# Kernel optimization log

Hardware: AMD Instinct MI355X
Metric: run time of the kernel (lower is better)

## Reference

```python
import jax, jax.numpy as jnp
import numpy as np

NPOINT = 2048

def setup_inputs() -> dict:
    key = jax.random.key(0)
    xyz = jax.random.normal(key, (32, 3, 65536), dtype=jnp.float32)
    return {"xyz": xyz}

def furthest_point_sampling(pts, npoint):
    # pts: [B, N, 3] -> indices [B, npoint] int32
    B, N, _ = pts.shape
    batch = jnp.arange(B)

    def step(carry, _):
        dist, farthest = carry  # dist [B,N], farthest [B]
        centroid = pts[batch, farthest]              # [B, 3]
        d = jnp.sum((pts - centroid[:, None, :]) ** 2, axis=-1)  # [B, N]
        dist = jnp.minimum(dist, d)
        nxt = jnp.argmax(dist, axis=-1).astype(jnp.int32)
        return (dist, nxt), farthest

    init = (jnp.full((B, N), 1e10, dtype=pts.dtype),
            jnp.zeros((B,), dtype=jnp.int32))
    _, idx = jax.lax.scan(step, init, None, length=npoint)
    return idx.T  # [B, npoint]

def reference(xyz):
    # xyz: [B, 3, N]; module permutes to [B, N, 3] and runs FPS
    pts = jnp.transpose(xyz, (0, 2, 1)).astype(jnp.float32)
    return furthest_point_sampling(pts, NPOINT)
```

## Files before the change

kernel.cpp:

```cpp
#include <hip/hip_runtime.h>
#include <stdint.h>

#pragma clang fp contract(off)

#define NPT      2048
#define NBATCH   32
#define NPTS     65536
#define MEMBERS  8
#define NTHREADS 512
#define CHUNK    (NPTS / MEMBERS)
#define PPT      (CHUNK / NTHREADS)
#define WPB      (NTHREADS / 64)

__device__ __forceinline__ uint32_t f2u(float f) { return __float_as_uint(f); }
__device__ __forceinline__ float u2f(uint32_t u) { return __uint_as_float(u); }

__global__ void __launch_bounds__(NTHREADS)
fps_kernel(const float* __restrict__ xyz, int* __restrict__ out,
           uint64_t* __restrict__ cand)
{
    __shared__ float    sx[CHUNK];
    __shared__ uint32_t red[WPB][2];
    __shared__ uint32_t bc[3];

    const int i = blockIdx.x;
    const int q = i >> 3;
    const int batch  = (i & 7) * 4 + (q & 3);
    const int member = q >> 2;
    const int tid  = threadIdx.x;
    const int lane = tid & 63;
    const int wv   = tid >> 6;

    const float* xb = xyz + (size_t)batch * 3 * NPTS;
    const int gbase = member * CHUNK;

    float py[PPT], pz[PPT], pd[PPT];
#pragma unroll
    for (int k = 0; k < PPT; ++k) {
        int p = tid + k * NTHREADS;
        int g = gbase + p;
        sx[p] = xb[g];
        py[k] = xb[NPTS + g];
        pz[k] = xb[2 * NPTS + g];
        pd[k] = 1e10f;
    }

    float cx = xb[0], cy = xb[NPTS], cz = xb[2 * NPTS];
    if (member == 0 && tid == 0) out[(size_t)batch * NPT] = 0;

    uint64_t* cb = cand + (size_t)batch * 2 * MEMBERS;

    for (int t = 0; t < NPT - 1; ++t) {
        float bv = -1.0f;
        int   bi = 0;
#pragma unroll
        for (int k = 0; k < PPT; ++k) {
            int p = tid + k * NTHREADS;
            float dx = sx[p] - cx;
            float dy = py[k] - cy;
            float dz = pz[k] - cz;
            float d  = dx * dx + dy * dy;
            d = d + dz * dz;
            float nd = fminf(pd[k], d);
            pd[k] = nd;
            bool g = nd > bv;
            bv = g ? nd : bv;
            bi = g ? (gbase + p) : bi;
        }

#pragma unroll
        for (int off = 1; off < 64; off <<= 1) {
            float ov = __shfl_xor(bv, off, 64);
            int   oi = __shfl_xor(bi, off, 64);
            if (ov > bv || (ov == bv && oi < bi)) { bv = ov; bi = oi; }
        }
        if (lane == 0) { red[wv][0] = f2u(bv); red[wv][1] = (uint32_t)bi; }
        __syncthreads();

        if (wv == 0) {
            float v = -1.0f; int ix = 0;
            if (lane < WPB) { v = u2f(red[lane][0]); ix = (int)red[lane][1]; }
#pragma unroll
            for (int off = 4; off >= 1; off >>= 1) {
                float ov = __shfl_xor(v, off, 64);
                int   oi = __shfl_xor(ix, off, 64);
                if (ov > v || (ov == v && oi < ix)) { v = ov; ix = oi; }
            }

            uint64_t* sb = cb + (size_t)(t & 1) * MEMBERS;
            const uint32_t tag = (uint32_t)t;
            if (lane == 0) {
                uint64_t w = ((uint64_t)f2u(v) << 32)
                           | (uint64_t)((uint32_t)ix << 16) | tag;
                __hip_atomic_store(&sb[member], w, __ATOMIC_RELAXED,
                                   __HIP_MEMORY_SCOPE_AGENT);
            }

            uint64_t w = 0; bool done = false;
            do {
                if (!done) w = __hip_atomic_load(&sb[lane & 7], __ATOMIC_RELAXED,
                                                 __HIP_MEMORY_SCOPE_AGENT);
                done = (uint32_t)(w & 0xFFFFu) == tag;
            } while (!__all(done));

            float gv = u2f((uint32_t)(w >> 32));
            int   gi = (int)((w >> 16) & 0xFFFFu);
#pragma unroll
            for (int off = 1; off < 8; off <<= 1) {
                float ov = __shfl_xor(gv, off, 64);
                int   oi = __shfl_xor(gi, off, 64);
                if (ov > gv || (ov == gv && oi < gi)) { gv = ov; gi = oi; }
            }

            if (lane < 3) bc[lane] = f2u(xb[(size_t)lane * NPTS + gi]);
            if (lane == 0 && member == 0) out[(size_t)batch * NPT + t + 1] = gi;
        }
        __syncthreads();
        cx = u2f(bc[0]); cy = u2f(bc[1]); cz = u2f(bc[2]);
    }
}

extern "C" void kernel_launch(void* const* d_in, const int* in_sizes, int n_in,
                              void* d_out, int out_size, void* d_ws, size_t ws_size,
                              hipStream_t stream)
{
    const float* xyz = (const float*)d_in[0];
    int* out = (int*)d_out;
    uint64_t* cand = (uint64_t*)d_ws;
    fps_kernel<<<NBATCH * MEMBERS, NTHREADS, 0, stream>>>(xyz, out, cand);
}
```

Baseline: 5.323 ms.

## Publish per-wave candidates globally and drop block barriers from FPS loop

```diff
diff --git a/kernel.cpp b/kernel.cpp
--- a/kernel.cpp
+++ b/kernel.cpp
@@ -11,17 +11,45 @@
 #define CHUNK    (NPTS / MEMBERS)
 #define PPT      (CHUNK / NTHREADS)
 #define WPB      (NTHREADS / 64)
+#define SLOTS    (MEMBERS * WPB)
 
 __device__ __forceinline__ uint32_t f2u(float f) { return __float_as_uint(f); }
 __device__ __forceinline__ float u2f(uint32_t u) { return __uint_as_float(u); }
 
-__global__ void __launch_bounds__(NTHREADS)
+__device__ __forceinline__ void amerge(float& v, int& i, float ov, int oi) {
+    if (ov > v || (ov == v && oi < i)) { v = ov; i = oi; }
+}
+
+template<int CTRL>
+__device__ __forceinline__ void dpp_round(float& v, int& i) {
+    float ov = u2f((uint32_t)__builtin_amdgcn_mov_dpp((int)f2u(v), CTRL, 0xf, 0xf, true));
+    int   oi = __builtin_amdgcn_mov_dpp(i, CTRL, 0xf, 0xf, true);
+    amerge(v, i, ov, oi);
+}
+__device__ __forceinline__ void swz16_round(float& v, int& i) {
+    float ov = u2f((uint32_t)__builtin_amdgcn_ds_swizzle((int)f2u(v), 0x401F));
+    int   oi = __builtin_amdgcn_ds_swizzle(i, 0x401F);
+    amerge(v, i, ov, oi);
+}
+__device__ __forceinline__ void shfl32_round(float& v, int& i) {
+    float ov = __shfl_xor(v, 32, 64);
+    int   oi = __shfl_xor(i, 32, 64);
+    amerge(v, i, ov, oi);
+}
+__device__ __forceinline__ void wave_argmax(float& v, int& i) {
+    dpp_round<0xB1>(v, i);
+    dpp_round<0x4E>(v, i);
+    dpp_round<0x141>(v, i);
+    dpp_round<0x140>(v, i);
+    swz16_round(v, i);
+    shfl32_round(v, i);
+}
+
+__global__ void __launch_bounds__(NTHREADS, 2)
 fps_kernel(const float* __restrict__ xyz, int* __restrict__ out,
            uint64_t* __restrict__ cand)
 {
-    __shared__ float    sx[CHUNK];
-    __shared__ uint32_t red[WPB][2];
-    __shared__ uint32_t bc[3];
+    __shared__ float sx[CHUNK];
 
     const int i = blockIdx.x;
     const int q = i >> 3;
@@ -48,7 +76,8 @@
     float cx = xb[0], cy = xb[NPTS], cz = xb[2 * NPTS];
     if (member == 0 && tid == 0) out[(size_t)batch * NPT] = 0;
 
-    uint64_t* cb = cand + (size_t)batch * 2 * MEMBERS;
+    uint64_t* cb = cand + (size_t)batch * 2 * SLOTS;
+    const int sid = member * WPB + wv;
 
     for (int t = 0; t < NPT - 1; ++t) {
         float bv = -1.0f;
@@ -68,55 +97,32 @@
             bi = g ? (gbase + p) : bi;
         }
 
-#pragma unroll
-        for (int off = 1; off < 64; off <<= 1) {
-            float ov = __shfl_xor(bv, off, 64);
-            int   oi = __shfl_xor(bi, off, 64);
-            if (ov > bv || (ov == bv && oi < bi)) { bv = ov; bi = oi; }
+        wave_argmax(bv, bi);
+
+        uint64_t* sb = cb + (size_t)(t & 1) * SLOTS;
+        const uint32_t tag = (uint32_t)t;
+        if (lane == 0) {
+            uint64_t w = ((uint64_t)f2u(bv) << 32)
+                       | ((uint64_t)(uint32_t)bi << 16) | tag;
+            __hip_atomic_store(&sb[sid], w, __ATOMIC_RELAXED,
+                               __HIP_MEMORY_SCOPE_AGENT);
         }
-        if (lane == 0) { red[wv][0] = f2u(bv); red[wv][1] = (uint32_t)bi; }
-        __syncthreads();
 
-        if (wv == 0) {
-            float v = -1.0f; int ix = 0;
-            if (lane < WPB) { v = u2f(red[lane][0]); ix = (int)red[lane][1]; }
-#pragma unroll
-            for (int off = 4; off >= 1; off >>= 1) {
-                float ov = __shfl_xor(v, off, 64);
-                int   oi = __shfl_xor(ix, off, 64);
-                if (ov > v || (ov == v && oi < ix)) { v = ov; ix = oi; }
-            }
+        uint64_t w = 0; bool done = false;
+        do {
+            if (!done) w = __hip_atomic_load(&sb[lane], __ATOMIC_RELAXED,
+                                             __HIP_MEMORY_SCOPE_AGENT);
+            done = (uint32_t)(w & 0xFFFFu) == tag;
+        } while (!__all(done));
 
-            uint64_t* sb = cb + (size_t)(t & 1) * MEMBERS;
-            const uint32_t tag = (uint32_t)t;
-            if (lane == 0) {
-                uint64_t w = ((uint64_t)f2u(v) << 32)
-                           | (uint64_t)((uint32_t)ix << 16) | tag;
-                __hip_atomic_store(&sb[member], w, __ATOMIC_RELAXED,
-                                   __HIP_MEMORY_SCOPE_AGENT);
-            }
+        float v  = u2f((uint32_t)(w >> 32));
+        int   gi = (int)((w >> 16) & 0xFFFFu);
+        wave_argmax(v, gi);
 
-            uint64_t w = 0; bool done = false;
-            do {
-                if (!done) w = __hip_atomic_load(&sb[lane & 7], __ATOMIC_RELAXED,
-                                                 __HIP_MEMORY_SCOPE_AGENT);
-                done = (uint32_t)(w & 0xFFFFu) == tag;
-            } while (!__all(done));
-
-            float gv = u2f((uint32_t)(w >> 32));
-            int   gi = (int)((w >> 16) & 0xFFFFu);
-#pragma unroll
-            for (int off = 1; off < 8; off <<= 1) {
-                float ov = __shfl_xor(gv, off, 64);
-                int   oi = __shfl_xor(gi, off, 64);
-                if (ov > gv || (ov == gv && oi < gi)) { gv = ov; gi = oi; }
-            }
-
-            if (lane < 3) bc[lane] = f2u(xb[(size_t)lane * NPTS + gi]);
-            if (lane == 0 && member == 0) out[(size_t)batch * NPT + t + 1] = gi;
-        }
-        __syncthreads();
-        cx = u2f(bc[0]); cy = u2f(bc[1]); cz = u2f(bc[2]);
+        cx = xb[gi];
+        cy = xb[NPTS + gi];
+        cz = xb[2 * NPTS + gi];
+        if (member == 0 && tid == 0) out[(size_t)batch * NPT + t + 1] = gi;
     }
 }
 
```

After: 11.34 ms. +113.1%, slower.
